# Optimization experiments

Hardware: AMD Instinct MI355X
Metric: run time of the kernel (lower is better)

Reference implementation:

```python
import jax, jax.numpy as jnp
import numpy as np

B, T, D, H, FF, L = 4, 2048, 512, 8, 2048, 4
IN_SIZE = 32
PAST, FUT = 128, 128
HD = D // H
EPS = 1e-5


def _layer_norm(x, g, b):
    m = jnp.mean(x, axis=-1, keepdims=True)
    v = jnp.mean((x - m) ** 2, axis=-1, keepdims=True)
    return (x - m) / jnp.sqrt(v + EPS) * g + b


def setup_inputs() -> dict:
    key = jax.random.key(0)
    ks = jax.random.split(key, 20)
    s = 0.02
    inp = {
        "beatmap_features": jax.random.normal(ks[0], (B, T, IN_SIZE), jnp.float32),
        "positions": jax.random.normal(ks[1], (B, T, 2), jnp.float32),
        "proj_w": jax.random.normal(ks[2], (D, IN_SIZE), jnp.float32) * s,
        "proj_b": jnp.zeros((D,), jnp.float32),
        "pos_enc": jax.random.normal(ks[3], (T, D), jnp.float32),
        # stacked per-layer params, leading dim L
        "qkv_w": jax.random.normal(ks[4], (L, 3 * D, D), jnp.float32) * s,
        "qkv_b": jnp.zeros((L, 3 * D), jnp.float32),
        "out_w": jax.random.normal(ks[5], (L, D, D), jnp.float32) * s,
        "out_b": jnp.zeros((L, D), jnp.float32),
        "ff1_w": jax.random.normal(ks[6], (L, FF, D), jnp.float32) * s,
        "ff1_b": jnp.zeros((L, FF), jnp.float32),
        "ff2_w": jax.random.normal(ks[7], (L, D, FF), jnp.float32) * s,
        "ff2_b": jnp.zeros((L, D), jnp.float32),
        "ln1_g": jnp.ones((L, D), jnp.float32),
        "ln1_b": jnp.zeros((L, D), jnp.float32),
        "ln2_g": jnp.ones((L, D), jnp.float32),
        "ln2_b": jnp.zeros((L, D), jnp.float32),
    }
    return inp


def reference(beatmap_features, positions, proj_w, proj_b, pos_enc,
              qkv_w, qkv_b, out_w, out_b, ff1_w, ff1_b, ff2_w, ff2_b,
              ln1_g, ln1_b, ln2_g, ln2_b):
    # positions only perturbed by noise during training; eval forward ignores it.
    x = beatmap_features @ proj_w.T + proj_b + pos_enc[None]  # [B,T,D]

    # banded local-window additive mask: allow j in [i-PAST, i+FUT]
    i = jnp.arange(T)[:, None]
    j = jnp.arange(T)[None, :]
    allow = (j >= i - PAST) & (j <= i + FUT)
    mask = jnp.where(allow, 0.0, -jnp.inf).astype(x.dtype)  # [T,T]

    scale = 1.0 / jnp.sqrt(jnp.asarray(HD, x.dtype))

    def enc_layer(x, p):
        qkvw, qkvb, ow, ob, f1w, f1b, f2w, f2b, g1, b1, g2, b2 = p
        qkv = x @ qkvw.T + qkvb                         # [B,T,3D]
        q, k, v = jnp.split(qkv, 3, axis=-1)
        q = q.reshape(B, T, H, HD).transpose(0, 2, 1, 3)  # [B,H,T,HD]
        k = k.reshape(B, T, H, HD).transpose(0, 2, 1, 3)
        v = v.reshape(B, T, H, HD).transpose(0, 2, 1, 3)
        scores = jnp.einsum('bhqd,bhkd->bhqk', q, k) * scale + mask
        attn = jax.nn.softmax(scores, axis=-1)
        o = jnp.einsum('bhqk,bhkd->bhqd', attn, v)
        o = o.transpose(0, 2, 1, 3).reshape(B, T, D) @ ow.T + ob
        x = _layer_norm(x + o, g1, b1)                  # post-norm (PyTorch default)
        h = jax.nn.relu(x @ f1w.T + f1b) @ f2w.T + f2b
        x = _layer_norm(x + h, g2, b2)
        return x, None

    params = (qkv_w, qkv_b, out_w, out_b, ff1_w, ff1_b, ff2_w, ff2_b,
              ln1_g, ln1_b, ln2_g, ln2_b)
    x, _ = jax.lax.scan(enc_layer, x, params)
    return x
```

## Files before the change

kernel.cpp:

```cpp
#include <hip/hip_runtime.h>
#include <hip/hip_bf16.h>

#define B_ 4
#define T_ 2048
#define D_ 512
#define H_ 8
#define FF_ 2048
#define L_ 4
#define NTOK 8192
#define EPS_ 1e-5f

typedef __hip_bfloat16 bf16;
typedef __attribute__((ext_vector_type(8))) short short8;
typedef __attribute__((ext_vector_type(4))) float floatx4;

__device__ __forceinline__ float bf2f(short s) {
    union { unsigned u; float f; } cv;
    cv.u = ((unsigned)(unsigned short)s) << 16;
    return cv.f;
}
__device__ __forceinline__ short f2bs(float f) {
    union { bf16 b; short s; } cv;
    cv.b = __float2bfloat16(f);
    return cv.s;
}

__global__ __launch_bounds__(256) void cvt_kernel(
    const float* __restrict__ in, bf16* __restrict__ out, int n4)
{
    int i = blockIdx.x * 256 + threadIdx.x;
    if (i >= n4) return;
    float4 v = ((const float4*)in)[i];
    out[i * 4 + 0] = __float2bfloat16(v.x);
    out[i * 4 + 1] = __float2bfloat16(v.y);
    out[i * 4 + 2] = __float2bfloat16(v.z);
    out[i * 4 + 3] = __float2bfloat16(v.w);
}

__global__ __launch_bounds__(256) void transpose_pw(
    const float* __restrict__ pw, float* __restrict__ pwT)
{
    int idx = blockIdx.x * 256 + threadIdx.x;
    int d = idx >> 5, k = idx & 31;
    pwT[k * D_ + d] = pw[idx];
}

__global__ __launch_bounds__(256) void proj_kernel(
    const float* __restrict__ feat, const float* __restrict__ pwT,
    const float* __restrict__ pb, const float* __restrict__ pe,
    float* __restrict__ x, bf16* __restrict__ xb)
{
    __shared__ float fs[16][32];
    int tok0 = blockIdx.x * 16;
    int tid = threadIdx.x;
    {
        float2 v = ((const float2*)(feat + (size_t)tok0 * 32))[tid];
        fs[tid >> 4][(tid & 15) * 2]     = v.x;
        fs[tid >> 4][(tid & 15) * 2 + 1] = v.y;
    }
    int d0 = tid * 2;
    float w0[32], w1[32];
    #pragma unroll
    for (int k = 0; k < 32; k++) {
        float2 wv = *(const float2*)(pwT + k * D_ + d0);
        w0[k] = wv.x; w1[k] = wv.y;
    }
    float2 pbv = *(const float2*)(pb + d0);
    __syncthreads();
    #pragma unroll 4
    for (int tok = 0; tok < 16; tok++) {
        int t = (tok0 + tok) & (T_ - 1);
        float s0 = pbv.x, s1 = pbv.y;
        #pragma unroll
        for (int k = 0; k < 32; k++) {
            float f = fs[tok][k];
            s0 += f * w0[k]; s1 += f * w1[k];
        }
        float2 pev = *(const float2*)(pe + (size_t)t * D_ + d0);
        s0 += pev.x; s1 += pev.y;
        size_t o = (size_t)(tok0 + tok) * D_ + d0;
        *(float2*)(x + o) = make_float2(s0, s1);
        union { struct { short a, b; } s; unsigned u; } pk;
        pk.s.a = f2bs(s0); pk.s.b = f2bs(s1);
        *(unsigned*)((short*)xb + o) = pk.u;
    }
}

template <int RELU>
__global__ __launch_bounds__(256) void gemm_bf16_kernel(
    const short* __restrict__ A, const short* __restrict__ W,
    const float* __restrict__ bias, bf16* __restrict__ Cb,
    int M, int N, int K)
{
    __shared__ __align__(16) short lds[128 * 136];
    int bm = blockIdx.y * 128, bn = blockIdx.x * 128;
    int tid = threadIdx.x;
    int w = tid >> 6, lane = tid & 63;
    int wm = (w >> 1) * 64, wn = (w & 1) * 64;

    floatx4 acc[4][4];
    #pragma unroll
    for (int i = 0; i < 4; i++)
        #pragma unroll
        for (int j = 0; j < 4; j++)
            acc[i][j] = (floatx4){0.f, 0.f, 0.f, 0.f};

    int srow = lane >> 2;
    int sslot = lane & 3;
    int lrow = lane & 15, lk = lane >> 4;

    auto issue = [&](int buf, int k0) {
        short* As = lds + buf * 4096;
        short* Bs = lds + 8192 + buf * 4096;
        #pragma unroll
        for (int inst = 0; inst < 2; inst++) {
            int r0 = w * 32 + inst * 16;
            int rA = r0 + srow;
            int cA = sslot ^ ((rA >> 1) & 3);
            const short* gA = A + (size_t)(bm + rA) * K + k0 + cA * 8;
            __builtin_amdgcn_global_load_lds(
                (const __attribute__((address_space(1))) void*)gA,
                (__attribute__((address_space(3))) void*)&As[r0 * 32], 16, 0, 0);
            const short* gB = W + (size_t)(bn + rA) * K + k0 + cA * 8;
            __builtin_amdgcn_global_load_lds(
                (const __attribute__((address_space(1))) void*)gB,
                (__attribute__((address_space(3))) void*)&Bs[r0 * 32], 16, 0, 0);
        }
    };

    int nIter = K >> 5;
    issue(0, 0);
    for (int it = 0; it < nIter; it++) {
        int buf = it & 1;
        __syncthreads();
        if (it + 1 < nIter) issue(buf ^ 1, (it + 1) * 32);

        const short* As = lds + buf * 4096;
        const short* Bs = lds + 8192 + buf * 4096;
        short8 af[4], bfr[4];
        #pragma unroll
        for (int i = 0; i < 4; i++) {
            int rr = wm + i * 16 + lrow;
            af[i] = *(const short8*)&As[rr * 32 + ((lk ^ ((rr >> 1) & 3)) * 8)];
            int nn = wn + i * 16 + lrow;
            bfr[i] = *(const short8*)&Bs[nn * 32 + ((lk ^ ((nn >> 1) & 3)) * 8)];
        }
        #pragma unroll
        for (int i = 0; i < 4; i++)
            #pragma unroll
            for (int j = 0; j < 4; j++)
                acc[i][j] = __builtin_amdgcn_mfma_f32_16x16x32_bf16(
                    af[i], bfr[j], acc[i][j], 0, 0, 0);
    }

    __syncthreads();

    int cl = lane & 15, rq = lane >> 4;
    #pragma unroll
    for (int i = 0; i < 4; i++) {
        #pragma unroll
        for (int j = 0; j < 4; j++) {
            int col = wn + j * 16 + cl;
            float bv = bias[bn + col];
            #pragma unroll
            for (int r = 0; r < 4; r++) {
                int row = wm + i * 16 + rq * 4 + r;
                float v = acc[i][j][r] + bv;
                if (RELU) v = fmaxf(v, 0.f);
                lds[row * 136 + col] = f2bs(v);
            }
        }
    }
    __syncthreads();

    #pragma unroll
    for (int s = 0; s < 8; s++) {
        int idx = tid + 256 * s;
        int r = idx >> 4, c8 = (idx & 15) * 8;
        short8 v = *(const short8*)&lds[r * 136 + c8];
        *(short8*)((short*)Cb + (size_t)(bm + r) * N + bn + c8) = v;
    }
}

__global__ __launch_bounds__(256, 4) void attn_kernel(
    const short* __restrict__ qkv, bf16* __restrict__ out)
{
    __shared__ __align__(16) short Qs[64 * 72];
    __shared__ __align__(16) short Ks[64 * 72];
    __shared__ __align__(16) short Vt[64 * 72];
    __shared__ __align__(16) short Ps[64 * 72];

    int q0 = blockIdx.x * 64;
    int bh = blockIdx.y;
    int b = bh >> 3, h = bh & 7;
    int tid = threadIdx.x;
    int w = tid >> 6, lane = tid & 63;
    int col = lane & 15, quad = lane >> 4;

    const size_t base = (size_t)b * T_ * 3 * D_;
    const int roww = 3 * D_;
    const int qoff = h * 64, koff = D_ + h * 64, voff = 2 * D_ + h * 64;

    #pragma unroll
    for (int i = 0; i < 2; i++) {
        int idx = tid + 256 * i;
        int r = idx >> 3, c8 = (idx & 7) * 8;
        *(short8*)&Qs[r * 72 + c8] =
            *(const short8*)(qkv + base + (size_t)(q0 + r) * roww + qoff + c8);
    }

    float l_r[4] = {0.f, 0.f, 0.f, 0.f};
    floatx4 Oacc[4];
    #pragma unroll
    for (int j = 0; j < 4; j++) Oacc[j] = (floatx4){0.f, 0.f, 0.f, 0.f};

    int klo = max(0, q0 - 128), khi = min(T_, q0 + 192);
    const float scale = 0.125f;
    int qrow = q0 + w * 16 + quad * 4;

    for (int kt = klo; kt < khi; kt += 64) {
        __syncthreads();
        #pragma unroll
        for (int i = 0; i < 2; i++) {
            int idx = tid + 256 * i;
            int r = idx >> 3, c8 = (idx & 7) * 8;
            *(short8*)&Ks[r * 72 + c8] =
                *(const short8*)(qkv + base + (size_t)(kt + r) * roww + koff + c8);
            short8 v = *(const short8*)(qkv + base + (size_t)(kt + r) * roww + voff + c8);
            #pragma unroll
            for (int u = 0; u < 8; u++) Vt[(c8 + u) * 72 + r] = v[u];
        }
        __syncthreads();

        short8 aq0 = *(const short8*)&Qs[(w * 16 + col) * 72 + quad * 8];
        short8 aq1 = *(const short8*)&Qs[(w * 16 + col) * 72 + 32 + quad * 8];
        floatx4 Sacc[4];
        #pragma unroll
        for (int j = 0; j < 4; j++) {
            short8 bk0 = *(const short8*)&Ks[(j * 16 + col) * 72 + quad * 8];
            short8 bk1 = *(const short8*)&Ks[(j * 16 + col) * 72 + 32 + quad * 8];
            floatx4 s = (floatx4){0.f, 0.f, 0.f, 0.f};
            s = __builtin_amdgcn_mfma_f32_16x16x32_bf16(aq0, bk0, s, 0, 0, 0);
            s = __builtin_amdgcn_mfma_f32_16x16x32_bf16(aq1, bk1, s, 0, 0, 0);
            Sacc[j] = s;
        }

        float ps[4] = {0.f, 0.f, 0.f, 0.f};
        #pragma unroll
        for (int j = 0; j < 4; j++) {
            int key = kt + j * 16 + col;
            #pragma unroll
            for (int r = 0; r < 4; r++) {
                int dj = key - (qrow + r);
                float p = (dj < -128 || dj > 128) ? 0.f : __expf(Sacc[j][r] * scale);
                ps[r] += p;
                Ps[(w * 16 + quad * 4 + r) * 72 + j * 16 + col] = f2bs(p);
            }
        }
        #pragma unroll
        for (int off = 1; off < 16; off <<= 1)
            #pragma unroll
            for (int r = 0; r < 4; r++)
                ps[r] += __shfl_xor(ps[r], off);
        #pragma unroll
        for (int r = 0; r < 4; r++) l_r[r] += ps[r];

        __syncthreads();

        short8 ap0 = *(const short8*)&Ps[(w * 16 + col) * 72 + quad * 8];
        short8 ap1 = *(const short8*)&Ps[(w * 16 + col) * 72 + 32 + quad * 8];
        #pragma unroll
        for (int j = 0; j < 4; j++) {
            short8 bv0 = *(const short8*)&Vt[(j * 16 + col) * 72 + quad * 8];
            short8 bv1 = *(const short8*)&Vt[(j * 16 + col) * 72 + 32 + quad * 8];
            Oacc[j] = __builtin_amdgcn_mfma_f32_16x16x32_bf16(ap0, bv0, Oacc[j], 0, 0, 0);
            Oacc[j] = __builtin_amdgcn_mfma_f32_16x16x32_bf16(ap1, bv1, Oacc[j], 0, 0, 0);
        }
    }

    float invl[4];
    #pragma unroll
    for (int r = 0; r < 4; r++) invl[r] = 1.0f / l_r[r];
    #pragma unroll
    for (int j = 0; j < 4; j++)
        #pragma unroll
        for (int r = 0; r < 4; r++)
            out[(size_t)(b * T_ + qrow + r) * D_ + h * 64 + j * 16 + col] =
                __float2bfloat16(Oacc[j][r] * invl[r]);
}

__global__ __launch_bounds__(256) void add_ln_kernel(
    const float* __restrict__ x, const short* __restrict__ delta,
    const float* __restrict__ g, const float* __restrict__ bta,
    float* __restrict__ out, bf16* __restrict__ outb)
{
    int wave = threadIdx.x >> 6, lane = threadIdx.x & 63;
    int row = blockIdx.x * 4 + wave;
    int c0 = lane * 8;
    const float* xr = x + (size_t)row * D_ + c0;
    float4 xa = *(const float4*)xr;
    float4 xc = *(const float4*)(xr + 4);
    short8 db = *(const short8*)(delta + (size_t)row * D_ + c0);
    float v[8];
    v[0] = xa.x + bf2f(db[0]); v[1] = xa.y + bf2f(db[1]);
    v[2] = xa.z + bf2f(db[2]); v[3] = xa.w + bf2f(db[3]);
    v[4] = xc.x + bf2f(db[4]); v[5] = xc.y + bf2f(db[5]);
    v[6] = xc.z + bf2f(db[6]); v[7] = xc.w + bf2f(db[7]);
    float s = 0.f;
    #pragma unroll
    for (int i = 0; i < 8; i++) s += v[i];
    #pragma unroll
    for (int off = 32; off > 0; off >>= 1) s += __shfl_xor(s, off);
    float mean = s * (1.0f / D_);
    float var = 0.f;
    #pragma unroll
    for (int i = 0; i < 8; i++) { float c = v[i] - mean; var += c * c; }
    #pragma unroll
    for (int off = 32; off > 0; off >>= 1) var += __shfl_xor(var, off);
    float inv = rsqrtf(var * (1.0f / D_) + EPS_);
    float4 g0 = *(const float4*)(g + c0), g1 = *(const float4*)(g + c0 + 4);
    float4 b0 = *(const float4*)(bta + c0), b1 = *(const float4*)(bta + c0 + 4);
    float o[8];
    o[0] = (v[0] - mean) * inv * g0.x + b0.x;
    o[1] = (v[1] - mean) * inv * g0.y + b0.y;
    o[2] = (v[2] - mean) * inv * g0.z + b0.z;
    o[3] = (v[3] - mean) * inv * g0.w + b0.w;
    o[4] = (v[4] - mean) * inv * g1.x + b1.x;
    o[5] = (v[5] - mean) * inv * g1.y + b1.y;
    o[6] = (v[6] - mean) * inv * g1.z + b1.z;
    o[7] = (v[7] - mean) * inv * g1.w + b1.w;
    float* orow = out + (size_t)row * D_ + c0;
    *(float4*)orow = make_float4(o[0], o[1], o[2], o[3]);
    *(float4*)(orow + 4) = make_float4(o[4], o[5], o[6], o[7]);
    short8 ob;
    #pragma unroll
    for (int i = 0; i < 8; i++) ob[i] = f2bs(o[i]);
    *(short8*)((short*)outb + (size_t)row * D_ + c0) = ob;
}

extern "C" void kernel_launch(void* const* d_in, const int* in_sizes, int n_in,
                              void* d_out, int out_size, void* d_ws, size_t ws_size,
                              hipStream_t stream)
{
    const float* feat    = (const float*)d_in[0];
    const float* proj_w  = (const float*)d_in[2];
    const float* proj_b  = (const float*)d_in[3];
    const float* pos_enc = (const float*)d_in[4];
    const float* qkv_w   = (const float*)d_in[5];
    const float* qkv_b   = (const float*)d_in[6];
    const float* out_w   = (const float*)d_in[7];
    const float* out_b   = (const float*)d_in[8];
    const float* ff1_w   = (const float*)d_in[9];
    const float* ff1_b   = (const float*)d_in[10];
    const float* ff2_w   = (const float*)d_in[11];
    const float* ff2_b   = (const float*)d_in[12];
    const float* ln1_g   = (const float*)d_in[13];
    const float* ln1_b   = (const float*)d_in[14];
    const float* ln2_g   = (const float*)d_in[15];
    const float* ln2_b   = (const float*)d_in[16];

    char* p = (char*)d_ws;
    float* x    = (float*)p;  p += (size_t)NTOK * D_ * 4;
    float* pwT  = (float*)p;  p += (size_t)32 * D_ * 4;
    bf16* tmp2b = (bf16*)p;   p += (size_t)NTOK * D_ * 2;
    bf16* xb    = (bf16*)p;   p += (size_t)NTOK * D_ * 2;
    bf16* qkvb  = (bf16*)p;   p += (size_t)NTOK * 3 * D_ * 2;
    bf16* hbuf  = (bf16*)p;   p += (size_t)NTOK * FF_ * 2;
    bf16* abuf  = (bf16*)p;   p += (size_t)NTOK * D_ * 2;
    bf16* wq    = (bf16*)p;   p += (size_t)L_ * 3 * D_ * D_ * 2;
    bf16* wo    = (bf16*)p;   p += (size_t)L_ * D_ * D_ * 2;
    bf16* w1    = (bf16*)p;   p += (size_t)L_ * FF_ * D_ * 2;
    bf16* w2    = (bf16*)p;   p += (size_t)L_ * D_ * FF_ * 2;
    float* outp = (float*)d_out;

    {
        int n4;
        n4 = L_ * 3 * D_ * D_ / 4; cvt_kernel<<<(n4 + 255) / 256, 256, 0, stream>>>(qkv_w, wq, n4);
        n4 = L_ * D_ * D_ / 4;     cvt_kernel<<<(n4 + 255) / 256, 256, 0, stream>>>(out_w, wo, n4);
        n4 = L_ * FF_ * D_ / 4;    cvt_kernel<<<(n4 + 255) / 256, 256, 0, stream>>>(ff1_w, w1, n4);
        n4 = L_ * D_ * FF_ / 4;    cvt_kernel<<<(n4 + 255) / 256, 256, 0, stream>>>(ff2_w, w2, n4);
        transpose_pw<<<64, 256, 0, stream>>>(proj_w, pwT);
    }

    proj_kernel<<<NTOK / 16, 256, 0, stream>>>(feat, pwT, proj_b, pos_enc, x, xb);

    for (int l = 0; l < L_; l++) {
        gemm_bf16_kernel<0><<<dim3(3 * D_ / 128, NTOK / 128), 256, 0, stream>>>(
            (const short*)xb, (const short*)(wq + (size_t)l * 3 * D_ * D_),
            qkv_b + (size_t)l * 3 * D_, qkvb, NTOK, 3 * D_, D_);
        attn_kernel<<<dim3(T_ / 64, B_ * H_), 256, 0, stream>>>((const short*)qkvb, abuf);
        gemm_bf16_kernel<0><<<dim3(D_ / 128, NTOK / 128), 256, 0, stream>>>(
            (const short*)abuf, (const short*)(wo + (size_t)l * D_ * D_),
            out_b + (size_t)l * D_, tmp2b, NTOK, D_, D_);
        add_ln_kernel<<<NTOK / 4, 256, 0, stream>>>(
            x, (const short*)tmp2b, ln1_g + (size_t)l * D_, ln1_b + (size_t)l * D_, x, xb);
        gemm_bf16_kernel<1><<<dim3(FF_ / 128, NTOK / 128), 256, 0, stream>>>(
            (const short*)xb, (const short*)(w1 + (size_t)l * FF_ * D_),
            ff1_b + (size_t)l * FF_, hbuf, NTOK, FF_, D_);
        gemm_bf16_kernel<0><<<dim3(D_ / 128, NTOK / 128), 256, 0, stream>>>(
            (const short*)hbuf, (const short*)(w2 + (size_t)l * D_ * FF_),
            ff2_b + (size_t)l * D_, tmp2b, NTOK, D_, FF_);
        float* dst = (l == L_ - 1) ? outp : x;
        add_ln_kernel<<<NTOK / 4, 256, 0, stream>>>(
            x, (const short*)tmp2b, ln2_g + (size_t)l * D_, ln2_b + (size_t)l * D_, dst, xb);
    }
}
```

Measured before the change: 709.1 us.

## Replace direct global-to-LDS loads with register-staged double-buffered prefetch in GEMM

The bf16 GEMM main loop no longer loads tiles with global_load_lds. It now stages tiles two k-steps ahead in registers and then writes them into alternating LDS buffers with ordinary vector stores, one barrier per half-step. The goal is deeper prefetch that hides global latency behind the MFMA work. In exchange it uses more VGPRs for the staged tiles and adds explicit LDS store instructions, which can lower occupancy. There is also a possible hazard: the same LDS buffer is overwritten two half-steps later with no barrier between the last read and the overwrite.

```diff
diff --git a/kernel.cpp b/kernel.cpp
--- a/kernel.cpp
+++ b/kernel.cpp
@@ -105,52 +105,70 @@
         for (int j = 0; j < 4; j++)
             acc[i][j] = (floatx4){0.f, 0.f, 0.f, 0.f};
 
-    int srow = lane >> 2;
-    int sslot = lane & 3;
+    int r0 = tid >> 2;
+    int c0 = tid & 3;
+    int slot = (c0 ^ ((r0 >> 1) & 3)) * 8;
+    const short* Arow0 = A + (size_t)(bm + r0) * K + c0 * 8;
+    const short* Arow1 = A + (size_t)(bm + r0 + 64) * K + c0 * 8;
+    const short* Brow0 = W + (size_t)(bn + r0) * K + c0 * 8;
+    const short* Brow1 = W + (size_t)(bn + r0 + 64) * K + c0 * 8;
+
     int lrow = lane & 15, lk = lane >> 4;
 
-    auto issue = [&](int buf, int k0) {
-        short* As = lds + buf * 4096;
-        short* Bs = lds + 8192 + buf * 4096;
-        #pragma unroll
-        for (int inst = 0; inst < 2; inst++) {
-            int r0 = w * 32 + inst * 16;
-            int rA = r0 + srow;
-            int cA = sslot ^ ((rA >> 1) & 3);
-            const short* gA = A + (size_t)(bm + rA) * K + k0 + cA * 8;
-            __builtin_amdgcn_global_load_lds(
-                (const __attribute__((address_space(1))) void*)gA,
-                (__attribute__((address_space(3))) void*)&As[r0 * 32], 16, 0, 0);
-            const short* gB = W + (size_t)(bn + rA) * K + k0 + cA * 8;
-            __builtin_amdgcn_global_load_lds(
-                (const __attribute__((address_space(1))) void*)gB,
-                (__attribute__((address_space(3))) void*)&Bs[r0 * 32], 16, 0, 0);
-        }
-    };
+    short8 ea0, ea1, eb0, eb1;
+    short8 oa0, oa1, ob0, ob1;
+    ea0 = *(const short8*)(Arow0);       ea1 = *(const short8*)(Arow1);
+    eb0 = *(const short8*)(Brow0);       eb1 = *(const short8*)(Brow1);
+    oa0 = *(const short8*)(Arow0 + 32);  oa1 = *(const short8*)(Arow1 + 32);
+    ob0 = *(const short8*)(Brow0 + 32);  ob1 = *(const short8*)(Brow1 + 32);
 
     int nIter = K >> 5;
-    issue(0, 0);
-    for (int it = 0; it < nIter; it++) {
-        int buf = it & 1;
-        __syncthreads();
-        if (it + 1 < nIter) issue(buf ^ 1, (it + 1) * 32);
-
-        const short* As = lds + buf * 4096;
-        const short* Bs = lds + 8192 + buf * 4096;
-        short8 af[4], bfr[4];
-        #pragma unroll
-        for (int i = 0; i < 4; i++) {
-            int rr = wm + i * 16 + lrow;
-            af[i] = *(const short8*)&As[rr * 32 + ((lk ^ ((rr >> 1) & 3)) * 8)];
-            int nn = wn + i * 16 + lrow;
-            bfr[i] = *(const short8*)&Bs[nn * 32 + ((lk ^ ((nn >> 1) & 3)) * 8)];
-        }
-        #pragma unroll
-        for (int i = 0; i < 4; i++)
-            #pragma unroll
-            for (int j = 0; j < 4; j++)
-                acc[i][j] = __builtin_amdgcn_mfma_f32_16x16x32_bf16(
-                    af[i], bfr[j], acc[i][j], 0, 0, 0);
+    for (int it = 0; it < nIter; it += 2) {
+        #pragma unroll
+        for (int half = 0; half < 2; half++) {
+            short* As = lds + half * 8192;
+            short* Bs = lds + half * 8192 + 4096;
+            if (half == 0) {
+                *(short8*)&As[r0 * 32 + slot] = ea0;
+                *(short8*)&As[(r0 + 64) * 32 + slot] = ea1;
+                *(short8*)&Bs[r0 * 32 + slot] = eb0;
+                *(short8*)&Bs[(r0 + 64) * 32 + slot] = eb1;
+            } else {
+                *(short8*)&As[r0 * 32 + slot] = oa0;
+                *(short8*)&As[(r0 + 64) * 32 + slot] = oa1;
+                *(short8*)&Bs[r0 * 32 + slot] = ob0;
+                *(short8*)&Bs[(r0 + 64) * 32 + slot] = ob1;
+            }
+            __syncthreads();
+            int kn = (it + half + 2) * 32;
+            if (kn < K) {
+                if (half == 0) {
+                    ea0 = *(const short8*)(Arow0 + kn);
+                    ea1 = *(const short8*)(Arow1 + kn);
+                    eb0 = *(const short8*)(Brow0 + kn);
+                    eb1 = *(const short8*)(Brow1 + kn);
+                } else {
+                    oa0 = *(const short8*)(Arow0 + kn);
+                    oa1 = *(const short8*)(Arow1 + kn);
+                    ob0 = *(const short8*)(Brow0 + kn);
+                    ob1 = *(const short8*)(Brow1 + kn);
+                }
+            }
+            short8 af[4], bfr[4];
+            #pragma unroll
+            for (int i = 0; i < 4; i++) {
+                int rr = wm + i * 16 + lrow;
+                af[i] = *(const short8*)&As[rr * 32 + ((lk ^ ((rr >> 1) & 3)) * 8)];
+                int nn = wn + i * 16 + lrow;
+                bfr[i] = *(const short8*)&Bs[nn * 32 + ((lk ^ ((nn >> 1) & 3)) * 8)];
+            }
+            #pragma unroll
+            for (int i = 0; i < 4; i++)
+                #pragma unroll
+                for (int j = 0; j < 4; j++)
+                    acc[i][j] = __builtin_amdgcn_mfma_f32_16x16x32_bf16(
+                        af[i], bfr[j], acc[i][j], 0, 0, 0);
+        }
     }
 
     __syncthreads();
```

Result: faster. 680.7 us (-4.0%).
